# Optimization experiments

Measured on AMD Instinct MI355X. Metric: run time of the kernel, lower is better.

Reference implementation:

```python
import jax, jax.numpy as jnp
import numpy as np

C, H, W = 8, 2048, 2048
NUM_SEG = 64      # labels 0..63; label 0 = background (ndimage.label convention)
SIGMA_AGG = 0.5


def setup_inputs() -> dict:
    key = jax.random.key(0)
    k1, k2, k3 = jax.random.split(key, 3)
    pred_similarities = jax.random.normal(k1, (C, H, W), dtype=jnp.float32)
    kernel_labels = jax.random.randint(k2, (H, W), 0, NUM_SEG).astype(jnp.int32)
    region_labels = jax.random.randint(k3, (H, W), 0, NUM_SEG).astype(jnp.int32)
    # masks are 1 exactly where a connected component exists (labels > 0),
    # matching what ndimage.label would produce from these masks
    kernels_mask = (kernel_labels > 0).astype(jnp.float32)
    regions_mask = (region_labels > 0).astype(jnp.float32)
    return {
        "pred_similarities": pred_similarities,
        "regions_mask": regions_mask,
        "kernels_mask": kernels_mask,
        "kernel_labels": kernel_labels,
        "region_labels": region_labels,
    }


def reference(pred_similarities, regions_mask, kernels_mask, kernel_labels, region_labels):
    h, w = kernel_labels.shape
    kl = kernel_labels.reshape(-1)  # [N]
    rl = region_labels.reshape(-1)  # [N]

    # per-label cardinality, broadcast back to pixels (label 0 contributes 0
    # because the mask is 0 there, matching the original's untouched zeros)
    kcard = jax.ops.segment_sum(kernels_mask.reshape(-1), kl, num_segments=NUM_SEG)[kl].reshape(h, w)
    rcard = jax.ops.segment_sum(regions_mask.reshape(-1), rl, num_segments=NUM_SEG)[rl].reshape(h, w)

    # per-channel, per-kernel-component sum of pred, broadcast back per pixel
    c = pred_similarities.shape[0]
    pred_flat = pred_similarities.reshape(c, -1)  # [C, N]
    seg = jax.vmap(lambda p: jax.ops.segment_sum(p, kl, num_segments=NUM_SEG))(pred_flat)  # [C, NUM_SEG]
    Gk = jnp.where(kl[None, :] > 0, seg[:, kl], 0.0).reshape(c, h, w)
    Gk = Gk / (kcard + 1.0)[None]

    Fp = pred_similarities * regions_mask[None]
    diff = Fp - Gk
    # torch.linalg.norm over the whole tensor -> scalar Frobenius norm
    D = jnp.maximum(jnp.sqrt(jnp.sum(diff * diff)) - SIGMA_AGG, 0.0)
    per_pixel = jnp.log(D * D + 1.0) / (rcard + 1.0)  # [H, W]

    num_region = jnp.maximum(jnp.max(region_labels), 1).astype(per_pixel.dtype)
    return jnp.sum(per_pixel) / num_region
```

## Files before the change

kernel.cpp:

```cpp
#include <hip/hip_runtime.h>
#include <math.h>

#define NPIX (2048*2048)
#define NBLOCKS 1024
#define CHUNK (NPIX/NBLOCKS)
#define SPX 256
#define NSTEP (CHUNK/SPX)
#define PSTR 260
#define KOFF (8*PSTR)
#define ROFF (KOFF+SPX)
#define SBUF (ROFF+SPX)
#define NBUF 3

#define WS_T1 1024
#define WS_T2 2048
#define WS_F2 2304
#define WS_FLOATS 2305
#define NREP 32
#define RSTRIDE 2432
#define L_T1 1088
#define L_T2 2176
#define LDS_RED (2176 + 16*17)

typedef __attribute__((ext_vector_type(8))) short short8;
typedef __attribute__((ext_vector_type(4))) float f32x4;
typedef __attribute__((ext_vector_type(4))) unsigned int u32x4;

typedef __attribute__((address_space(3))) unsigned int lds_uint;
typedef __attribute__((address_space(1))) unsigned int glb_uint;

#define WAITVM(n) __builtin_amdgcn_s_waitcnt(0x0F70 | (n))

__device__ __forceinline__ unsigned int pk_trunc_bf16(float lo, float hi) {
    return __builtin_amdgcn_perm(__float_as_uint(hi), __float_as_uint(lo), 0x07060302u);
}
__device__ __forceinline__ unsigned int pk_lab(int lo, int hi) {
    return __builtin_amdgcn_perm((unsigned)hi, (unsigned)lo, 0x05040100u);
}
__device__ __forceinline__ unsigned int onehot2(unsigned int x, unsigned int tp) {
    const unsigned int a = x ^ tp;
    const unsigned int t = 0x40004000u - a;
    return t & 0x40004000u;
}

__device__ __forceinline__ void dma1k(const void* g, void* l, int lane) {
    __builtin_amdgcn_global_load_lds(
        (const glb_uint*)((const char*)g + lane * 16),
        (lds_uint*)l, 16, 0, 0);
}

__device__ __forceinline__ void issue_dma(int wv, int lane, float* base, int P,
                                          const float* pred, const int* kl,
                                          const int* rl) {
    dma1k(pred + (size_t)wv * NPIX + P,      base + wv * PSTR,      lane);
    dma1k(pred + (size_t)(wv + 4) * NPIX + P, base + (wv + 4) * PSTR, lane);
    if (wv == 0) dma1k(kl + P, base + KOFF, lane);
    if (wv == 1) dma1k(rl + P, base + ROFF, lane);
}

__global__ __launch_bounds__(256, 4) void agg_mfma(
    const float* __restrict__ pred,
    const int*   __restrict__ kl,
    const int*   __restrict__ rl,
    float* __restrict__ ws)
{
    __shared__ union {
        float stage[NBUF][SBUF];
        float red[LDS_RED];
    } sh;
    __shared__ float s_f2w[4];

    const int tid  = threadIdx.x;
    const int wv   = tid >> 6;
    const int lane = tid & 63;
    const int quad = lane >> 4;
    const int col  = lane & 15;
    const int c8   = col & 7;
    const bool lowcol = (col < 8);
    const unsigned int cpack = (unsigned)col * 0x00010001u;
    const unsigned int tps[4] = {cpack, cpack + 0x00100010u,
                                 cpack + 0x00200020u, cpack + 0x00300030u};
    const unsigned int hc = (col == 8) ? 0x3F803F80u : 0u;
    const short8 b2c = __builtin_bit_cast(short8, (u32x4){hc, hc, hc, hc});

    f32x4 acc0[4], acc1[4], acc2;
    #pragma unroll
    for (int s = 0; s < 4; ++s) {
        acc0[s] = (f32x4){0.f, 0.f, 0.f, 0.f};
        acc1[s] = (f32x4){0.f, 0.f, 0.f, 0.f};
    }
    acc2 = (f32x4){0.f, 0.f, 0.f, 0.f};
    float f2 = 0.f;

    const int P0 = blockIdx.x * CHUNK;
    issue_dma(wv, lane, sh.stage[0], P0,       pred, kl, rl);
    issue_dma(wv, lane, sh.stage[1], P0 + SPX, pred, kl, rl);

    int cur = 0;
    for (int s = 0; s < NSTEP; ++s) {
        int pf = cur + 2; if (pf >= NBUF) pf -= NBUF;
        if (s + 2 < NSTEP)
            issue_dma(wv, lane, sh.stage[pf], P0 + (s + 2) * SPX, pred, kl, rl);
        if (s + 2 < NSTEP)      { if (wv < 2) WAITVM(6); else WAITVM(4); }
        else if (s + 1 < NSTEP) { if (wv < 2) WAITVM(3); else WAITVM(2); }
        else                    WAITVM(0);
        __builtin_amdgcn_s_barrier();

        const float* base = sh.stage[cur];
        #pragma unroll
        for (int i = 0; i < 2; ++i) {
            const int pb = (2 * wv + i) * 32 + quad * 8;
            const int* kptr = (const int*)(base + KOFF) + pb;
            const int* rptr = (const int*)(base + ROFF) + pb;
            const float* pptr = base + c8 * PSTR + pb;
            const int4 ka = *(const int4*)kptr;
            const int4 kb = *(const int4*)(kptr + 4);
            const int4 ra = *(const int4*)rptr;
            const int4 rb = *(const int4*)(rptr + 4);
            const float4 pa = *(const float4*)pptr;
            const float4 pb4 = *(const float4*)(pptr + 4);

            const int   klv[8] = {ka.x, ka.y, ka.z, ka.w, kb.x, kb.y, kb.z, kb.w};
            const int   rlv[8] = {ra.x, ra.y, ra.z, ra.w, rb.x, rb.y, rb.z, rb.w};
            const float pv[8]  = {pa.x, pa.y, pa.z, pa.w, pb4.x, pb4.y, pb4.z, pb4.w};

            float pr[8];
            #pragma unroll
            for (int j = 0; j < 8; ++j) {
                pr[j] = (rlv[j] > 0) ? pv[j] : 0.f;
                f2 = fmaf(pr[j], pr[j], f2);
            }
            unsigned int b1p[4], kp[4], rp[4];
            #pragma unroll
            for (int q = 0; q < 4; ++q) {
                const int j0 = 2 * q, j1 = 2 * q + 1;
                const unsigned int plo = pk_trunc_bf16(pv[j0], pv[j1]);
                const unsigned int phi = pk_trunc_bf16(pr[j0], pr[j1]);
                b1p[q] = lowcol ? plo : phi;
                kp[q]  = pk_lab(klv[j0], klv[j1]);
                rp[q]  = pk_lab(rlv[j0], rlv[j1]);
            }
            const short8 b1 = __builtin_bit_cast(short8,
                (u32x4){b1p[0], b1p[1], b1p[2], b1p[3]});

            #pragma unroll
            for (int t = 0; t < 4; ++t) {
                u32x4 oh;
                #pragma unroll
                for (int q = 0; q < 4; ++q) oh[q] = onehot2(kp[q], tps[t]);
                const short8 ak = __builtin_bit_cast(short8, oh);
                acc0[t] = __builtin_amdgcn_mfma_f32_16x16x32_bf16(ak, b1,  acc0[t], 0, 0, 0);
                acc1[t] = __builtin_amdgcn_mfma_f32_16x16x32_bf16(ak, b2c, acc1[t], 0, 0, 0);
            }
            u32x4 alo, bhi;
            #pragma unroll
            for (int q = 0; q < 4; ++q) {
                alo[q] = onehot2(rp[q] & 0x000F000Fu, cpack);
                bhi[q] = onehot2((rp[q] >> 4) & 0x00030003u, cpack);
            }
            acc2 = __builtin_amdgcn_mfma_f32_16x16x32_bf16(
                __builtin_bit_cast(short8, alo), __builtin_bit_cast(short8, bhi),
                acc2, 0, 0, 0);
        }
        __builtin_amdgcn_s_barrier();
        ++cur; if (cur == NBUF) cur = 0;
    }

    #pragma unroll
    for (int off = 32; off > 0; off >>= 1) f2 += __shfl_down(f2, off, 64);
    if (lane == 0) s_f2w[wv] = f2;

    __syncthreads();
    for (int w = 0; w < 4; ++w) {
        if (wv == w) {
            #pragma unroll
            for (int t = 0; t < 4; ++t)
                #pragma unroll
                for (int i = 0; i < 4; ++i) {
                    const int l = t * 16 + quad * 4 + i;
                    const int a0 = l * 17 + col;
                    const int a1 = L_T1 + l * 17 + col;
                    if (w == 0) { sh.red[a0] = acc0[t][i]; sh.red[a1] = acc1[t][i]; }
                    else        { sh.red[a0] += acc0[t][i]; sh.red[a1] += acc1[t][i]; }
                }
            #pragma unroll
            for (int i = 0; i < 4; ++i) {
                const int a2 = L_T2 + (quad * 4 + i) * 17 + col;
                if (w == 0) sh.red[a2] = acc2[i]; else sh.red[a2] += acc2[i];
            }
        }
        __syncthreads();
    }
    float* wsr = ws + (size_t)(blockIdx.x & (NREP - 1)) * RSTRIDE;
    if (tid == 0)
        atomicAdd(&wsr[WS_F2], s_f2w[0] + s_f2w[1] + s_f2w[2] + s_f2w[3]);
    for (int idx = tid; idx < 2304; idx += 256) {
        int a;
        if (idx < 1024)      a = (idx >> 4) * 17 + (idx & 15);
        else if (idx < 2048) a = L_T1 + ((idx - 1024) >> 4) * 17 + (idx & 15);
        else                 a = L_T2 + ((idx - 2048) >> 4) * 17 + (idx & 15);
        atomicAdd(&wsr[idx], sh.red[a]);
    }
}

__global__ __launch_bounds__(256) void agg_reduce(float* __restrict__ ws)
{
    const int i = blockIdx.x * 256 + threadIdx.x;
    if (i >= WS_FLOATS) return;
    float s = ws[i];
    #pragma unroll 4
    for (int r = 1; r < NREP; ++r) s += ws[i + (size_t)r * RSTRIDE];
    ws[i] = s;
}

__global__ __launch_bounds__(64) void agg_final(const float* __restrict__ ws,
                                                float* __restrict__ out)
{
    const int l = threadIdx.x;
    const float* t0 = ws + l * 16;
    const float pck = 0.5f  * ws[WS_T1 + l * 16 + 8];
    const float pcr = 0.25f * ws[WS_T2 + (l & 15) * 16 + (l >> 4)];

    float corr = 0.f;
    if (l > 0) {
        #pragma unroll
        for (int c = 0; c < 8; ++c) {
            const float seg = 0.5f * t0[c];
            const float T   = 0.5f * t0[8 + c];
            const float gk  = seg / (pck + 1.f);
            corr += gk * (gk * pck - 2.f * T);
        }
    }
    const float rcard = (l > 0) ? pcr : 0.f;
    float S = pcr / (rcard + 1.f);
    int mx = (pcr > 0.5f) ? l : 0;
    float f2 = (l == 0) ? 0.5f * ws[WS_F2] : 0.f;

    #pragma unroll
    for (int off = 32; off > 0; off >>= 1) {
        f2   += __shfl_down(f2, off, 64);
        corr += __shfl_down(corr, off, 64);
        S    += __shfl_down(S, off, 64);
        mx    = max(mx, __shfl_down(mx, off, 64));
    }
    if (l == 0) {
        const float SS = f2 + corr;
        float D = sqrtf(fmaxf(SS, 0.f)) - 0.5f;
        D = fmaxf(D, 0.f);
        out[0] = logf(D * D + 1.f) * S / (float)max(mx, 1);
    }
}

extern "C" void kernel_launch(void* const* d_in, const int* in_sizes, int n_in,
                              void* d_out, int out_size, void* d_ws, size_t ws_size,
                              hipStream_t stream) {
    const float* pred = (const float*)d_in[0];
    const int* kl = (const int*)d_in[3];
    const int* rl = (const int*)d_in[4];
    float* ws = (float*)d_ws;

    hipMemsetAsync(d_ws, 0, (size_t)NREP * RSTRIDE * sizeof(float), stream);
    agg_mfma<<<NBLOCKS, 256, 0, stream>>>(pred, kl, rl, ws);
    agg_reduce<<<(WS_FLOATS + 255) / 256, 256, 0, stream>>>(ws);
    agg_final<<<1, 64, 0, stream>>>(ws, (float*)d_out);
}
```

Measured before the change: 263.4 us.

## Replace LDS DMA staging pipeline with direct global vector loads

Removes the triple-buffered global_load_lds staging through shared memory and its per-step barriers. Each lane now reads its pred, kernel-label and region-label vectors straight from global memory, with the step loop unrolled. This is meant to cut barrier and waitcnt stalls and free LDS for higher occupancy. The cost is redundant per-lane loads of the same addresses, which lean on the cache, and the loss of explicit prefetching.

```diff
diff --git a/kernel.cpp b/kernel.cpp
--- a/kernel.cpp
+++ b/kernel.cpp
@@ -6,11 +6,6 @@
 #define CHUNK (NPIX/NBLOCKS)
 #define SPX 256
 #define NSTEP (CHUNK/SPX)
-#define PSTR 260
-#define KOFF (8*PSTR)
-#define ROFF (KOFF+SPX)
-#define SBUF (ROFF+SPX)
-#define NBUF 3
 
 #define WS_T1 1024
 #define WS_T2 2048
@@ -26,11 +21,6 @@
 typedef __attribute__((ext_vector_type(4))) float f32x4;
 typedef __attribute__((ext_vector_type(4))) unsigned int u32x4;
 
-typedef __attribute__((address_space(3))) unsigned int lds_uint;
-typedef __attribute__((address_space(1))) unsigned int glb_uint;
-
-#define WAITVM(n) __builtin_amdgcn_s_waitcnt(0x0F70 | (n))
-
 __device__ __forceinline__ unsigned int pk_trunc_bf16(float lo, float hi) {
     return __builtin_amdgcn_perm(__float_as_uint(hi), __float_as_uint(lo), 0x07060302u);
 }
@@ -41,21 +31,6 @@
     const unsigned int a = x ^ tp;
     const unsigned int t = 0x40004000u - a;
     return t & 0x40004000u;
-}
-
-__device__ __forceinline__ void dma1k(const void* g, void* l, int lane) {
-    __builtin_amdgcn_global_load_lds(
-        (const glb_uint*)((const char*)g + lane * 16),
-        (lds_uint*)l, 16, 0, 0);
-}
-
-__device__ __forceinline__ void issue_dma(int wv, int lane, float* base, int P,
-                                          const float* pred, const int* kl,
-                                          const int* rl) {
-    dma1k(pred + (size_t)wv * NPIX + P,      base + wv * PSTR,      lane);
-    dma1k(pred + (size_t)(wv + 4) * NPIX + P, base + (wv + 4) * PSTR, lane);
-    if (wv == 0) dma1k(kl + P, base + KOFF, lane);
-    if (wv == 1) dma1k(rl + P, base + ROFF, lane);
 }
 
 __global__ __launch_bounds__(256, 4) void agg_mfma(
@@ -64,10 +39,7 @@
     const int*   __restrict__ rl,
     float* __restrict__ ws)
 {
-    __shared__ union {
-        float stage[NBUF][SBUF];
-        float red[LDS_RED];
-    } sh;
+    __shared__ float red[LDS_RED];
     __shared__ float s_f2w[4];
 
     const int tid  = threadIdx.x;
@@ -93,32 +65,22 @@
     float f2 = 0.f;
 
     const int P0 = blockIdx.x * CHUNK;
-    issue_dma(wv, lane, sh.stage[0], P0,       pred, kl, rl);
-    issue_dma(wv, lane, sh.stage[1], P0 + SPX, pred, kl, rl);
-
-    int cur = 0;
+    const int pbase = (2 * wv) * 32 + quad * 8;
+    const float* pp = pred + (size_t)c8 * NPIX + P0 + pbase;
+    const int*   kp = kl + P0 + pbase;
+    const int*   rp = rl + P0 + pbase;
+
+    #pragma unroll 4
     for (int s = 0; s < NSTEP; ++s) {
-        int pf = cur + 2; if (pf >= NBUF) pf -= NBUF;
-        if (s + 2 < NSTEP)
-            issue_dma(wv, lane, sh.stage[pf], P0 + (s + 2) * SPX, pred, kl, rl);
-        if (s + 2 < NSTEP)      { if (wv < 2) WAITVM(6); else WAITVM(4); }
-        else if (s + 1 < NSTEP) { if (wv < 2) WAITVM(3); else WAITVM(2); }
-        else                    WAITVM(0);
-        __builtin_amdgcn_s_barrier();
-
-        const float* base = sh.stage[cur];
         #pragma unroll
         for (int i = 0; i < 2; ++i) {
-            const int pb = (2 * wv + i) * 32 + quad * 8;
-            const int* kptr = (const int*)(base + KOFF) + pb;
-            const int* rptr = (const int*)(base + ROFF) + pb;
-            const float* pptr = base + c8 * PSTR + pb;
-            const int4 ka = *(const int4*)kptr;
-            const int4 kb = *(const int4*)(kptr + 4);
-            const int4 ra = *(const int4*)rptr;
-            const int4 rb = *(const int4*)(rptr + 4);
-            const float4 pa = *(const float4*)pptr;
-            const float4 pb4 = *(const float4*)(pptr + 4);
+            const int off = s * SPX + i * 32;
+            const float4 pa  = *(const float4*)(pp + off);
+            const float4 pb4 = *(const float4*)(pp + off + 4);
+            const int4   ka  = *(const int4*)(kp + off);
+            const int4   kb  = *(const int4*)(kp + off + 4);
+            const int4   ra  = *(const int4*)(rp + off);
+            const int4   rb  = *(const int4*)(rp + off + 4);
 
             const int   klv[8] = {ka.x, ka.y, ka.z, ka.w, kb.x, kb.y, kb.z, kb.w};
             const int   rlv[8] = {ra.x, ra.y, ra.z, ra.w, rb.x, rb.y, rb.z, rb.w};
@@ -130,15 +92,15 @@
                 pr[j] = (rlv[j] > 0) ? pv[j] : 0.f;
                 f2 = fmaf(pr[j], pr[j], f2);
             }
-            unsigned int b1p[4], kp[4], rp[4];
+            unsigned int b1p[4], kp4[4], rp4[4];
             #pragma unroll
             for (int q = 0; q < 4; ++q) {
                 const int j0 = 2 * q, j1 = 2 * q + 1;
                 const unsigned int plo = pk_trunc_bf16(pv[j0], pv[j1]);
                 const unsigned int phi = pk_trunc_bf16(pr[j0], pr[j1]);
                 b1p[q] = lowcol ? plo : phi;
-                kp[q]  = pk_lab(klv[j0], klv[j1]);
-                rp[q]  = pk_lab(rlv[j0], rlv[j1]);
+                kp4[q] = pk_lab(klv[j0], klv[j1]);
+                rp4[q] = pk_lab(rlv[j0], rlv[j1]);
             }
             const short8 b1 = __builtin_bit_cast(short8,
                 (u32x4){b1p[0], b1p[1], b1p[2], b1p[3]});
@@ -147,7 +109,7 @@
             for (int t = 0; t < 4; ++t) {
                 u32x4 oh;
                 #pragma unroll
-                for (int q = 0; q < 4; ++q) oh[q] = onehot2(kp[q], tps[t]);
+                for (int q = 0; q < 4; ++q) oh[q] = onehot2(kp4[q], tps[t]);
                 const short8 ak = __builtin_bit_cast(short8, oh);
                 acc0[t] = __builtin_amdgcn_mfma_f32_16x16x32_bf16(ak, b1,  acc0[t], 0, 0, 0);
                 acc1[t] = __builtin_amdgcn_mfma_f32_16x16x32_bf16(ak, b2c, acc1[t], 0, 0, 0);
@@ -155,15 +117,13 @@
             u32x4 alo, bhi;
             #pragma unroll
             for (int q = 0; q < 4; ++q) {
-                alo[q] = onehot2(rp[q] & 0x000F000Fu, cpack);
-                bhi[q] = onehot2((rp[q] >> 4) & 0x00030003u, cpack);
+                alo[q] = onehot2(rp4[q] & 0x000F000Fu, cpack);
+                bhi[q] = onehot2((rp4[q] >> 4) & 0x00030003u, cpack);
             }
             acc2 = __builtin_amdgcn_mfma_f32_16x16x32_bf16(
                 __builtin_bit_cast(short8, alo), __builtin_bit_cast(short8, bhi),
                 acc2, 0, 0, 0);
         }
-        __builtin_amdgcn_s_barrier();
-        ++cur; if (cur == NBUF) cur = 0;
     }
 
     #pragma unroll
@@ -180,13 +140,13 @@
                     const int l = t * 16 + quad * 4 + i;
                     const int a0 = l * 17 + col;
                     const int a1 = L_T1 + l * 17 + col;
-                    if (w == 0) { sh.red[a0] = acc0[t][i]; sh.red[a1] = acc1[t][i]; }
-                    else        { sh.red[a0] += acc0[t][i]; sh.red[a1] += acc1[t][i]; }
+                    if (w == 0) { red[a0] = acc0[t][i]; red[a1] = acc1[t][i]; }
+                    else        { red[a0] += acc0[t][i]; red[a1] += acc1[t][i]; }
                 }
             #pragma unroll
             for (int i = 0; i < 4; ++i) {
                 const int a2 = L_T2 + (quad * 4 + i) * 17 + col;
-                if (w == 0) sh.red[a2] = acc2[i]; else sh.red[a2] += acc2[i];
+                if (w == 0) red[a2] = acc2[i]; else red[a2] += acc2[i];
             }
         }
         __syncthreads();
@@ -199,7 +159,7 @@
         if (idx < 1024)      a = (idx >> 4) * 17 + (idx & 15);
         else if (idx < 2048) a = L_T1 + ((idx - 1024) >> 4) * 17 + (idx & 15);
         else                 a = L_T2 + ((idx - 2048) >> 4) * 17 + (idx & 15);
-        atomicAdd(&wsr[idx], sh.red[a]);
+        atomicAdd(&wsr[idx], red[a]);
     }
 }
 
```

Result: no change. 258.3 us (-2.0%).
